# Optimization experiments

Hardware: AMD Instinct MI355X
Metric: run time of the kernel (lower is better)

The kernel has to match this reference:

```python
import jax, jax.numpy as jnp
import numpy as np

B, S, D = 4, 2048, 2048
H, G, HD = 16, 4, 128  # n_heads, kv groups, head_dim
EPS = 1e-6


def setup_inputs() -> dict:
    key = jax.random.key(0)
    ks = jax.random.split(key, 8)
    x = jax.random.normal(ks[0], (B, S, D), dtype=jnp.float32)
    # causal mask, True = attend (already 'inverted' for SDPA semantics)
    mask = jnp.tril(jnp.ones((S, S), dtype=bool))
    # RoPE tables: (S, HD), rotate-half convention with duplicated freqs
    inv_freq = 1.0 / (10000.0 ** (np.arange(0, HD, 2, dtype=np.float32) / HD))
    ang = np.arange(S, dtype=np.float32)[:, None] * inv_freq[None, :]  # (S, HD/2)
    ang = np.concatenate([ang, ang], axis=-1)  # (S, HD)
    cos = jnp.asarray(np.cos(ang))
    sin = jnp.asarray(np.sin(ang))
    s = 0.02
    wq = jax.random.normal(ks[1], (D, H * HD), dtype=jnp.float32) * s
    wk = jax.random.normal(ks[2], (D, G * HD), dtype=jnp.float32) * s
    wv = jax.random.normal(ks[3], (D, G * HD), dtype=jnp.float32) * s
    wg = jax.random.normal(ks[4], (D, H * HD), dtype=jnp.float32) * s
    wo = jax.random.normal(ks[5], (H * HD, D), dtype=jnp.float32) * s
    q_scale = jax.random.normal(ks[6], (HD,), dtype=jnp.float32) * 0.01  # zero-centered
    k_scale = jax.random.normal(ks[7], (HD,), dtype=jnp.float32) * 0.01
    return dict(x=x, mask=mask, cos=cos, sin=sin, wq=wq, wk=wk, wv=wv,
                wg=wg, wo=wo, q_scale=q_scale, k_scale=k_scale)


def _zc_rmsnorm(x, scale):
    # zero-centered RMSNorm in fp32: x * rsqrt(mean(x^2)+eps) * (1+scale)
    xf = x.astype(jnp.float32)
    rms = jax.lax.rsqrt(jnp.mean(xf * xf, axis=-1, keepdims=True) + EPS)
    return (xf * rms * (1.0 + scale)).astype(x.dtype)


def _rope(x, cos, sin):
    # x: (b, h, s, hd); cos/sin: (s, hd)
    hd = x.shape[-1]
    x1, x2 = x[..., : hd // 2], x[..., hd // 2 :]
    rot = jnp.concatenate([-x2, x1], axis=-1)
    return x * cos[None, None] + rot * sin[None, None]


def reference(x, mask, cos, sin, wq, wk, wv, wg, wo, q_scale, k_scale):
    b, s, d = x.shape
    q = (x @ wq).reshape(b, s, H, HD).transpose(0, 2, 1, 3)   # (b,H,s,hd)
    k = (x @ wk).reshape(b, s, G, HD).transpose(0, 2, 1, 3)   # (b,G,s,hd)
    v = (x @ wv).reshape(b, s, G, HD).transpose(0, 2, 1, 3)
    gate = jax.nn.sigmoid(x @ wg)                              # (b,s,H*HD)

    q = _rope(_zc_rmsnorm(q, q_scale), cos, sin)
    k = _rope(_zc_rmsnorm(k, k_scale), cos, sin)

    rep = H // G
    k = jnp.repeat(k, rep, axis=1)   # (b,H,s,hd)
    v = jnpep = jnp.repeat(v, rep, axis=1) if False else jnp.repeat(v, rep, axis=1)

    scores = jnp.einsum('bhqd,bhkd->bhqk', q, k) / jnp.sqrt(jnp.float32(HD))
    scores = jnp.where(mask[None, None, :s, :s], scores, jnp.float32(-1e30))
    attn = jax.nn.softmax(scores, axis=-1)
    ctx = jnp.einsum('bhqk,bhkd->bhqd', attn, v)               # (b,H,s,hd)
    ctx = ctx.transpose(0, 2, 1, 3).reshape(b, s, H * HD)
    return (ctx * gate) @ wo
```

## Files before the change

kernel.cpp:

```cpp
#include <hip/hip_runtime.h>

typedef __bf16 bf16;
typedef __attribute__((ext_vector_type(8))) __bf16 bf16x8;
typedef __attribute__((ext_vector_type(4))) float f32x4;

constexpr int Bb = 4, S = 2048, Dd = 2048, H = 16, G = 4, HD = 128;
constexpr float L2E = 1.4426950408889634f;

__device__ inline f32x4 mfma16(bf16x8 a, bf16x8 b, f32x4 c) {
  return __builtin_amdgcn_mfma_f32_16x16x32_bf16(a, b, c, 0, 0, 0);
}

__device__ inline void gl_lds16(const void* g, void* l) {
  __builtin_amdgcn_global_load_lds(
      (const __attribute__((address_space(1))) void*)g,
      (__attribute__((address_space(3))) void*)l, 16, 0, 0);
}

__global__ __launch_bounds__(256) void k_f32_to_bf16(
    const float* __restrict__ in, bf16* __restrict__ out, int n8) {
  int i = blockIdx.x * 256 + threadIdx.x;
  if (i >= n8) return;
  const float4* p = (const float4*)(in + (long long)i * 8);
  float4 a = p[0], b = p[1];
  bf16x8 v;
  v[0] = (bf16)a.x; v[1] = (bf16)a.y; v[2] = (bf16)a.z; v[3] = (bf16)a.w;
  v[4] = (bf16)b.x; v[5] = (bf16)b.y; v[6] = (bf16)b.z; v[7] = (bf16)b.w;
  *(bf16x8*)(out + (long long)i * 8) = v;
}

__global__ __launch_bounds__(256) void k_wtrans(
    const float* __restrict__ wq, const float* __restrict__ wk,
    const float* __restrict__ wv, const float* __restrict__ wg,
    const float* __restrict__ wo, bf16* __restrict__ wcat,
    bf16* __restrict__ woT) {
  __shared__ float tile[32][33];
  const int z = blockIdx.z;
  const float* src;
  bf16* dst;
  int C;
  switch (z) {
    case 0: src = wq; C = 2048; dst = wcat; break;
    case 1: src = wk; C = 512; dst = wcat + (long long)2048 * 2048; break;
    case 2: src = wv; C = 512; dst = wcat + (long long)2560 * 2048; break;
    case 3: src = wg; C = 2048; dst = wcat + (long long)3072 * 2048; break;
    default: src = wo; C = 2048; dst = woT; break;
  }
  int c0 = blockIdx.x * 32, r0 = blockIdx.y * 32;
  if (c0 >= C) return;
  int tx = threadIdx.x, ty = threadIdx.y;
#pragma unroll
  for (int i = 0; i < 4; ++i) {
    int r = r0 + ty + i * 8, c = c0 + tx;
    tile[ty + i * 8][tx] = (c < C) ? src[(long long)r * C + c] : 0.f;
  }
  __syncthreads();
#pragma unroll
  for (int i = 0; i < 4; ++i) {
    int c = c0 + ty + i * 8, r = r0 + tx;
    if (c < C) dst[(long long)c * 2048 + r] = (bf16)tile[tx][ty + i * 8];
  }
}

template <typename InT>
__global__ __launch_bounds__(256) void k_transpose_bf16(
    const InT* __restrict__ in, long long s1, int nb2, long long s2, int ldin,
    bf16* __restrict__ out, long long obatch, int ldout, int R, int C) {
  __shared__ float tile[32][33];
  int z = blockIdx.z;
  const InT* ip = in + (long long)(z / nb2) * s1 + (long long)(z % nb2) * s2;
  bf16* op = out + (long long)z * obatch;
  int c0 = blockIdx.x * 32, r0 = blockIdx.y * 32;
  int tx = threadIdx.x, ty = threadIdx.y;
#pragma unroll
  for (int i = 0; i < 4; ++i) {
    int r = r0 + ty + i * 8, c = c0 + tx;
    tile[ty + i * 8][tx] = (r < R && c < C) ? (float)ip[(long long)r * ldin + c] : 0.f;
  }
  __syncthreads();
#pragma unroll
  for (int i = 0; i < 4; ++i) {
    int c = c0 + ty + i * 8, r = r0 + tx;
    if (c < C && r < R) op[(long long)c * ldout + r] = (bf16)tile[tx][ty + i * 8];
  }
}

template <typename CT, bool SIG>
__global__ __launch_bounds__(512, 1) void k_gemm256(
    const bf16* __restrict__ A, int lda, const bf16* __restrict__ Bt, int ldb,
    CT* __restrict__ C, int ldc, int M, int N, int K, int sig_from) {
  __shared__ bf16 ldsbuf[65536];
  char* lds2 = (char*)ldsbuf;
  const int tid = threadIdx.x;
  const int w = tid >> 6, lane = tid & 63;
  const int l16 = lane & 15, lh = lane >> 4;
  const int wr = w >> 2, wc = w & 3;
  const int nbn = N >> 8;
  const int cpx = gridDim.x >> 3;
  const int swz = (blockIdx.x & 7) * cpx + (blockIdx.x >> 3);
  const int bm = swz / nbn, bn = swz % nbn;
  const int m0 = bm << 8, n0 = bn << 8;

  const int lrow = lane >> 3;
  const int lcol = ((lane & 7) ^ lrow) * 8;
  const int arb = wr * 128 + wc * 16;
  const int xg = wc >> 1, sg = wr * 2 + (wc & 1);
  const int brb = xg * 128 + (sg >> 1) * 64 + (sg & 1) * 16;
  const bf16* aS0 = A + (long long)(m0 + arb + lrow) * lda + lcol;
  const bf16* aS1 = A + (long long)(m0 + arb + 8 + lrow) * lda + lcol;
  const bf16* bS0 = Bt + (long long)(n0 + brb + lrow) * ldb + lcol;
  const bf16* bS1 = Bt + (long long)(n0 + brb + 8 + lrow) * ldb + lcol;

  auto stageA = [&](int buf, int k0, int hi) {
    k0 = (k0 < K) ? k0 : 0;
    gl_lds16(aS0 + (long long)hi * 64 * lda + k0,
             lds2 + buf * 65536 + (arb + hi * 64) * 128);
    gl_lds16(aS1 + (long long)hi * 64 * lda + k0,
             lds2 + buf * 65536 + (arb + hi * 64 + 8) * 128);
  };
  auto stageB = [&](int buf, int k0, int hi) {
    k0 = (k0 < K) ? k0 : 0;
    gl_lds16(bS0 + (long long)hi * 32 * ldb + k0,
             lds2 + buf * 65536 + 32768 + (brb + hi * 32) * 128);
    gl_lds16(bS1 + (long long)hi * 32 * ldb + k0,
             lds2 + buf * 65536 + 32768 + (brb + hi * 32 + 8) * 128);
  };

  const int swzc = (l16 & 7) << 4;
  auto rdA = [&](bf16x8 (&dst)[4][2], const char* L, int mh) {
#pragma unroll
    for (int m = 0; m < 4; ++m)
#pragma unroll
      for (int ks = 0; ks < 2; ++ks)
        dst[m][ks] = *(const bf16x8*)(L + (wr * 128 + mh * 64 + m * 16 + l16) * 128 +
                                      ((ks * 64 + lh * 16) ^ swzc));
  };
  auto rdB = [&](bf16x8 (&dst)[2][2], const char* L, int nh) {
#pragma unroll
    for (int n = 0; n < 2; ++n)
#pragma unroll
      for (int ks = 0; ks < 2; ++ks)
        dst[n][ks] = *(const bf16x8*)(L + 32768 + (wc * 64 + nh * 32 + n * 16 + l16) * 128 +
                                      ((ks * 64 + lh * 16) ^ swzc));
  };

  f32x4 acc[8][4] = {};
  bf16x8 aflo[4][2], afhi[4][2], bn0[2][2], bn1[2][2];
  const int NT = K >> 6;

  stageA(0, 0, 0);
  stageB(0, 0, 0);
  stageB(0, 0, 1);
  stageA(0, 0, 1);
  stageA(1, 64, 0);
  asm volatile("s_waitcnt vmcnt(4)" ::: "memory");
  __builtin_amdgcn_s_barrier();
  asm volatile("" ::: "memory");
  rdA(aflo, lds2, 0);
  rdB(bn0, lds2, 0);

  for (int t = 0; t < NT; ++t) {
    const int buf = t & 1, nb = buf ^ 1;
    const char* L = lds2 + buf * 65536;
    const char* Ln = lds2 + nb * 65536;
    const int k1 = (t + 1) << 6;
    const bool more = (t + 1 < NT);
    stageB(nb, k1, 0);
    rdB(bn1, L, 1);
    __builtin_amdgcn_s_setprio(1);
#pragma unroll
    for (int ks = 0; ks < 2; ++ks)
#pragma unroll
      for (int m = 0; m < 4; ++m)
#pragma unroll
        for (int n = 0; n < 2; ++n)
          acc[m][n] = mfma16(aflo[m][ks], bn0[n][ks], acc[m][n]);
    __builtin_amdgcn_s_setprio(0);
    asm volatile("s_waitcnt vmcnt(4)" ::: "memory");
    __builtin_amdgcn_s_barrier();
    asm volatile("" ::: "memory");
    stageB(nb, k1, 1);
    rdA(afhi, L, 1);
    __builtin_amdgcn_s_setprio(1);
#pragma unroll
    for (int ks = 0; ks < 2; ++ks)
#pragma unroll
      for (int m = 0; m < 4; ++m)
#pragma unroll
        for (int n = 0; n < 2; ++n)
          acc[m][2 + n] = mfma16(aflo[m][ks], bn1[n][ks], acc[m][2 + n]);
    __builtin_amdgcn_s_setprio(0);
    __builtin_amdgcn_s_barrier();
    asm volatile("" ::: "memory");
    stageA(nb, k1, 1);
    __builtin_amdgcn_s_setprio(1);
#pragma unroll
    for (int ks = 0; ks < 2; ++ks)
#pragma unroll
      for (int m = 0; m < 4; ++m)
#pragma unroll
        for (int n = 0; n < 2; ++n)
          acc[4 + m][2 + n] = mfma16(afhi[m][ks], bn1[n][ks], acc[4 + m][2 + n]);
    __builtin_amdgcn_s_setprio(0);
    asm volatile("s_waitcnt vmcnt(4)" ::: "memory");
    __builtin_amdgcn_s_barrier();
    asm volatile("" ::: "memory");
    if (more) rdA(aflo, Ln, 0);
    stageA(buf, (t + 2) << 6, 0);
    __builtin_amdgcn_s_setprio(1);
#pragma unroll
    for (int ks = 0; ks < 2; ++ks)
#pragma unroll
      for (int m = 0; m < 4; ++m)
#pragma unroll
        for (int n = 0; n < 2; ++n)
          acc[4 + m][n] = mfma16(afhi[m][ks], bn0[n][ks], acc[4 + m][n]);
    __builtin_amdgcn_s_setprio(0);
    if (more) rdB(bn0, Ln, 0);
    asm volatile("s_waitcnt vmcnt(4)" ::: "memory");
    __builtin_amdgcn_s_barrier();
    asm volatile("" ::: "memory");
  }

#pragma unroll
  for (int m = 0; m < 8; ++m)
#pragma unroll
    for (int n = 0; n < 4; ++n) {
      const int col = n0 + wc * 64 + n * 16 + l16;
#pragma unroll
      for (int r = 0; r < 4; ++r) {
        float v = acc[m][n][r];
        if (SIG && col >= sig_from) v = 1.f / (1.f + exp2f(-v * L2E));
        C[(long long)(m0 + wr * 128 + m * 16 + lh * 4 + r) * ldc + col] = (CT)v;
      }
    }
}

__global__ __launch_bounds__(256) void k_rms_rope2(
    const bf16* __restrict__ C1, const float* __restrict__ qs,
    const float* __restrict__ ksc, const float* __restrict__ cosT,
    const float* __restrict__ sinT, bf16* __restrict__ qb,
    bf16* __restrict__ kb) {
  int wid = (blockIdx.x * 256 + threadIdx.x) >> 6;
  int lane = threadIdx.x & 63;
  const bf16* ip;
  const float* scale;
  bf16* op;
  float oscale;
  int s;
  if (wid < 131072) {
    int h = wid & 15, bs = wid >> 4;
    s = bs & 2047;
    int b = bs >> 11;
    ip = C1 + (long long)bs * 5120 + h * HD;
    scale = qs;
    oscale = 0.12751879523209308f;
    op = qb + (((long long)b * H + h) * S + s) * HD;
  } else {
    wid -= 131072;
    int h = wid & 3, bs = wid >> 2;
    s = bs & 2047;
    int b = bs >> 11;
    ip = C1 + 2048 + (long long)bs * 5120 + h * HD;
    scale = ksc;
    oscale = 1.0f;
    op = kb + (((long long)b * G + h) * S + s) * HD;
  }
  float x1 = (float)ip[lane], x2 = (float)ip[lane + 64];
  float ss = x1 * x1 + x2 * x2;
#pragma unroll
  for (int m = 1; m < 64; m <<= 1) ss += __shfl_xor(ss, m);
  float rms = rsqrtf(ss * (1.f / 128.f) + 1e-6f);
  float n1 = x1 * rms * (1.f + scale[lane]);
  float n2 = x2 * rms * (1.f + scale[lane + 64]);
  float o1 = (n1 * cosT[s * 128 + lane] - n2 * sinT[s * 128 + lane]) * oscale;
  float o2 = (n2 * cosT[s * 128 + lane + 64] + n1 * sinT[s * 128 + lane + 64]) * oscale;
  op[lane] = (bf16)o1;
  op[lane + 64] = (bf16)o2;
}

__global__ __launch_bounds__(512, 2) void k_flash3(
    const bf16* __restrict__ Q, const bf16* __restrict__ Kb,
    const bf16* __restrict__ Vt, const bf16* __restrict__ gate, int ldg,
    bf16* __restrict__ outc, int ldo) {
  __shared__ bf16 Ks[2][64 * 128];
  __shared__ bf16 Vs[128 * 64];
  __shared__ bf16 Ps[8][32 * 64];
  const int tid = threadIdx.x, w = tid >> 6, lane = tid & 63;
  const int l16 = lane & 15, lh = lane >> 4;
  const int bh = blockIdx.x & 63;
  const int qi = blockIdx.x >> 6;
  const int qc = 7 - qi;
  const int h = bh & 15, b = bh >> 4, g = h >> 2;
  const int qbase = qc * 256;
  const int q0w = qbase + w * 32;
  const bf16* qp = Q + (((long long)b * H + h) * S + q0w) * HD;
  const bf16* kp = Kb + ((long long)b * G + g) * S * HD;
  const bf16* vp = Vt + ((long long)b * G + g) * (long long)HD * S;

  bf16x8 aq[2][4];
#pragma unroll
  for (int m = 0; m < 2; ++m)
#pragma unroll
    for (int ks = 0; ks < 4; ++ks)
      aq[m][ks] = *(const bf16x8*)(qp + (long long)(m * 16 + l16) * HD + ks * 32 + lh * 8);

  f32x4 acc[2][8] = {};
  float mrow[2][4], lrow[2][4];
#pragma unroll
  for (int m = 0; m < 2; ++m)
#pragma unroll
    for (int r = 0; r < 4; ++r) { mrow[m][r] = -1e30f; lrow[m][r] = 0.f; }

  const int ntiles = qc * 4 + 4;

  auto stageK = [&](int bi, int t) {
    const int kv0 = t << 6;
#pragma unroll
    for (int i = 0; i < 2; ++i) {
      int c = w * 128 + i * 64 + lane;
      int row = c >> 4;
      int cb = ((c & 15) << 4) ^ ((row & 7) << 4);
      gl_lds16(kp + (long long)(kv0 + row) * HD + (cb >> 1),
               (char*)Ks[bi] + (w * 128 + i * 64) * 16);
    }
  };
  auto stageV = [&](int t) {
    const int kv0 = t << 6;
#pragma unroll
    for (int i = 0; i < 2; ++i) {
      int c = w * 128 + i * 64 + lane;
      int rowv = c >> 3;
      int cbv = ((c & 7) << 4) ^ ((rowv & 7) << 4);
      gl_lds16(vp + (long long)rowv * S + kv0 + (cbv >> 1),
               (char*)Vs + (w * 128 + i * 64) * 16);
    }
  };

  stageK(0, 0);
  asm volatile("s_waitcnt vmcnt(0)" ::: "memory");
  __builtin_amdgcn_s_barrier();
  asm volatile("" ::: "memory");

  for (int t = 0; t < ntiles; ++t) {
    const int buf = t & 1;
    const int kv0 = t << 6;
    const bool active = (kv0 <= q0w + 31);
    stageV(t);
    if (t + 1 < ntiles) stageK(buf ^ 1, t + 1);
    if (active) {
      f32x4 s[2][4] = {};
#pragma unroll
      for (int ks = 0; ks < 4; ++ks)
#pragma unroll
        for (int n = 0; n < 4; ++n) {
          int row = n * 16 + l16;
          int off = row * 256 + ((ks * 64 + lh * 16) ^ ((row & 7) << 4));
          bf16x8 kb = *(const bf16x8*)((const char*)Ks[buf] + off);
#pragma unroll
          for (int m = 0; m < 2; ++m) s[m][n] = mfma16(aq[m][ks], kb, s[m][n]);
        }
      if (kv0 + 63 > q0w) {
#pragma unroll
        for (int m = 0; m < 2; ++m)
#pragma unroll
          for (int n = 0; n < 4; ++n)
#pragma unroll
            for (int r = 0; r < 4; ++r) {
              int col = kv0 + n * 16 + l16;
              int rowg = q0w + m * 16 + lh * 4 + r;
              if (col > rowg) s[m][n][r] = -1e30f;
            }
      }
      float lm[2][4];
      bool okl = true;
#pragma unroll
      for (int m = 0; m < 2; ++m)
#pragma unroll
        for (int r = 0; r < 4; ++r) {
          lm[m][r] = fmaxf(fmaxf(s[m][0][r], s[m][1][r]), fmaxf(s[m][2][r], s[m][3][r]));
          okl = okl && (lm[m][r] <= mrow[m][r] + 8.f);
        }
      if (!__all(okl)) {
#pragma unroll
        for (int st = 1; st < 16; st <<= 1)
#pragma unroll
          for (int m = 0; m < 2; ++m)
#pragma unroll
            for (int r = 0; r < 4; ++r) lm[m][r] = fmaxf(lm[m][r], __shfl_xor(lm[m][r], st));
#pragma unroll
        for (int m = 0; m < 2; ++m)
#pragma unroll
          for (int r = 0; r < 4; ++r) {
            float mn = fmaxf(mrow[m][r], lm[m][r]);
            float resc = exp2f(mrow[m][r] - mn);
            mrow[m][r] = mn;
            lrow[m][r] *= resc;
#pragma unroll
            for (int dt = 0; dt < 8; ++dt) acc[m][dt][r] *= resc;
          }
      }
#pragma unroll
      for (int m = 0; m < 2; ++m)
#pragma unroll
        for (int n = 0; n < 4; ++n)
#pragma unroll
          for (int r = 0; r < 4; ++r) {
            float p = exp2f(s[m][n][r] - mrow[m][r]);
            s[m][n][r] = p;
            int row = m * 16 + lh * 4 + r;
            *(bf16*)((char*)Ps[w] + row * 128 +
                     ((n * 32 + l16 * 2) ^ ((row & 7) << 4))) = (bf16)p;
          }
#pragma unroll
      for (int m = 0; m < 2; ++m)
#pragma unroll
        for (int r = 0; r < 4; ++r)
          lrow[m][r] += s[m][0][r] + s[m][1][r] + s[m][2][r] + s[m][3][r];
    }
    asm volatile("s_waitcnt vmcnt(2)" ::: "memory");
    __builtin_amdgcn_s_barrier();
    asm volatile("" ::: "memory");
    if (active) {
      bf16x8 pa[2][2];
#pragma unroll
      for (int m = 0; m < 2; ++m)
#pragma unroll
        for (int kf = 0; kf < 2; ++kf) {
          int row = m * 16 + l16;
          pa[m][kf] = *(const bf16x8*)((const char*)Ps[w] + row * 128 +
                                       ((kf * 64 + lh * 16) ^ ((row & 7) << 4)));
        }
#pragma unroll
      for (int kf = 0; kf < 2; ++kf)
#pragma unroll
        for (int dt = 0; dt < 8; ++dt) {
          int d = dt * 16 + l16;
          int off = d * 128 + ((kf * 64 + lh * 16) ^ ((d & 7) << 4));
          bf16x8 vb = *(const bf16x8*)((const char*)Vs + off);
#pragma unroll
          for (int m = 0; m < 2; ++m) acc[m][dt] = mfma16(pa[m][kf], vb, acc[m][dt]);
        }
    }
    asm volatile("s_waitcnt vmcnt(0)" ::: "memory");
    __builtin_amdgcn_s_barrier();
    asm volatile("" ::: "memory");
  }

#pragma unroll
  for (int st = 1; st < 16; st <<= 1)
#pragma unroll
    for (int m = 0; m < 2; ++m)
#pragma unroll
      for (int r = 0; r < 4; ++r) lrow[m][r] += __shfl_xor(lrow[m][r], st);
  float inv[2][4];
#pragma unroll
  for (int m = 0; m < 2; ++m)
#pragma unroll
    for (int r = 0; r < 4; ++r) inv[m][r] = 1.f / lrow[m][r];
#pragma unroll
  for (int m = 0; m < 2; ++m)
#pragma unroll
    for (int dt = 0; dt < 8; ++dt)
#pragma unroll
      for (int r = 0; r < 4; ++r) {
        int rowg = q0w + m * 16 + lh * 4 + r;
        long long row = (long long)b * S + rowg;
        int col = h * HD + dt * 16 + l16;
        float gv = (float)gate[row * ldg + col];
        outc[row * ldo + col] = (bf16)(acc[m][dt][r] * inv[m][r] * gv);
      }
}

extern "C" void kernel_launch(void* const* d_in, const int* in_sizes, int n_in,
                              void* d_out, int out_size, void* d_ws, size_t ws_size,
                              hipStream_t stream) {
  const float* x = (const float*)d_in[0];
  const float* cosT = (const float*)d_in[2];
  const float* sinT = (const float*)d_in[3];
  const float* wq = (const float*)d_in[4];
  const float* wk = (const float*)d_in[5];
  const float* wv = (const float*)d_in[6];
  const float* wg = (const float*)d_in[7];
  const float* wo = (const float*)d_in[8];
  const float* qs = (const float*)d_in[9];
  const float* ksc = (const float*)d_in[10];
  float* out = (float*)d_out;
  char* ws = (char*)d_ws;

  if (ws_size < 146800640) return;
  bf16* xb = (bf16*)(ws);
  bf16* wcat = (bf16*)(ws + 33554432);
  bf16* woT = (bf16*)(ws + 54525952);
  bf16* C1 = (bf16*)(ws + 62914560);
  bf16* qbuf = xb;
  bf16* kbuf = wcat;
  bf16* vtbuf = wcat + 4194304;
  bf16* gatep = C1 + 3072;
  bf16* ctxg = C1;

  dim3 tb(32, 8);
  k_f32_to_bf16<<<8192, 256, 0, stream>>>(x, xb, Bb * S * Dd / 8);
  k_wtrans<<<dim3(64, 64, 5), tb, 0, stream>>>(wq, wk, wv, wg, wo, wcat, woT);
  k_gemm256<bf16, true><<<32 * 20, 512, 0, stream>>>(
      xb, 2048, wcat, 2048, C1, 5120, 8192, 5120, 2048, 3072);
  k_rms_rope2<<<40960, 256, 0, stream>>>(C1, qs, ksc, cosT, sinT, qbuf, kbuf);
  k_transpose_bf16<bf16><<<dim3(4, 64, 16), tb, 0, stream>>>(
      C1 + 2560, (long long)2048 * 5120, 4, 128, 5120, vtbuf,
      (long long)128 * 2048, 2048, 2048, 128);
  k_flash3<<<512, 512, 0, stream>>>(qbuf, kbuf, vtbuf, gatep, 5120, ctxg, 5120);
  k_gemm256<float, false><<<32 * 8, 512, 0, stream>>>(
      ctxg, 5120, woT, 2048, out, 2048, 8192, 2048, 2048, 1 << 30);
}
```

Measured before the change: 443.2 us.

## Restructure GEMM main loop into unrolled two-tile ping-pong with explicit LDS waits

Rewrites the 256x256 bf16 GEMM K-loop as a macro-expanded stage sequence, unrolled by two so the LDS buffer offsets are compile-time constants. It also reorders the global-to-LDS stage issue, LDS fragment reads and barriers, using lgkmcnt waits and sched_barrier to separate memory phases from MFMA clusters. The aim is to cut per-iteration address arithmetic and branches and to overlap loads with MFMA work more tightly. The tail handling assumes an even tile count of at least two, and the added barriers and waits could stall the waves.

```diff
diff --git a/kernel.cpp b/kernel.cpp
--- a/kernel.cpp
+++ b/kernel.cpp
@@ -111,116 +111,116 @@
   const bf16* bS0 = Bt + (long long)(n0 + brb + lrow) * ldb + lcol;
   const bf16* bS1 = Bt + (long long)(n0 + brb + 8 + lrow) * ldb + lcol;
 
-  auto stageA = [&](int buf, int k0, int hi) {
-    k0 = (k0 < K) ? k0 : 0;
+  auto stageA = [&](int bufoff, int k0, int hi) {
     gl_lds16(aS0 + (long long)hi * 64 * lda + k0,
-             lds2 + buf * 65536 + (arb + hi * 64) * 128);
+             lds2 + bufoff + (arb + hi * 64) * 128);
     gl_lds16(aS1 + (long long)hi * 64 * lda + k0,
-             lds2 + buf * 65536 + (arb + hi * 64 + 8) * 128);
-  };
-  auto stageB = [&](int buf, int k0, int hi) {
-    k0 = (k0 < K) ? k0 : 0;
+             lds2 + bufoff + (arb + hi * 64 + 8) * 128);
+  };
+  auto stageB = [&](int bufoff, int k0, int hi) {
     gl_lds16(bS0 + (long long)hi * 32 * ldb + k0,
-             lds2 + buf * 65536 + 32768 + (brb + hi * 32) * 128);
+             lds2 + bufoff + 32768 + (brb + hi * 32) * 128);
     gl_lds16(bS1 + (long long)hi * 32 * ldb + k0,
-             lds2 + buf * 65536 + 32768 + (brb + hi * 32 + 8) * 128);
+             lds2 + bufoff + 32768 + (brb + hi * 32 + 8) * 128);
   };
 
   const int swzc = (l16 & 7) << 4;
-  auto rdA = [&](bf16x8 (&dst)[4][2], const char* L, int mh) {
+  auto rdA = [&](bf16x8 (&dst)[4][2], int bufoff, int mh) {
 #pragma unroll
     for (int m = 0; m < 4; ++m)
 #pragma unroll
       for (int ks = 0; ks < 2; ++ks)
-        dst[m][ks] = *(const bf16x8*)(L + (wr * 128 + mh * 64 + m * 16 + l16) * 128 +
+        dst[m][ks] = *(const bf16x8*)(lds2 + bufoff +
+                                      (wr * 128 + mh * 64 + m * 16 + l16) * 128 +
                                       ((ks * 64 + lh * 16) ^ swzc));
   };
-  auto rdB = [&](bf16x8 (&dst)[2][2], const char* L, int nh) {
+  auto rdB = [&](bf16x8 (&dst)[2][2], int bufoff, int nh) {
 #pragma unroll
     for (int n = 0; n < 2; ++n)
 #pragma unroll
       for (int ks = 0; ks < 2; ++ks)
-        dst[n][ks] = *(const bf16x8*)(L + 32768 + (wc * 64 + nh * 32 + n * 16 + l16) * 128 +
+        dst[n][ks] = *(const bf16x8*)(lds2 + bufoff + 32768 +
+                                      (wc * 64 + nh * 32 + n * 16 + l16) * 128 +
                                       ((ks * 64 + lh * 16) ^ swzc));
   };
 
   f32x4 acc[8][4] = {};
   bf16x8 aflo[4][2], afhi[4][2], bn0[2][2], bn1[2][2];
+
+  auto mmc = [&](const bf16x8 (&AF)[4][2], const bf16x8 (&BF)[2][2], int MB, int NB) {
+#pragma unroll
+    for (int ks = 0; ks < 2; ++ks)
+#pragma unroll
+      for (int m = 0; m < 4; ++m)
+#pragma unroll
+        for (int n = 0; n < 2; ++n)
+          acc[MB + m][NB + n] = mfma16(AF[m][ks], BF[n][ks], acc[MB + m][NB + n]);
+  };
+
   const int NT = K >> 6;
+
+#define KTILE(CUR, NXT, KA, KB)                                         \
+  {                                                                     \
+                      \
+    rdA(aflo, CUR, 0);                                                  \
+    rdB(bn0, CUR, 0);                                                   \
+    stageB(NXT, KA, 1);                                                 \
+    asm volatile("s_waitcnt lgkmcnt(8)" ::: "memory");                  \
+    __builtin_amdgcn_s_barrier();                                       \
+    asm volatile("s_waitcnt lgkmcnt(0)" ::: "memory");                  \
+    __builtin_amdgcn_sched_barrier(0);                                  \
+    __builtin_amdgcn_s_setprio(1);                                      \
+    mmc(aflo, bn0, 0, 0);                                               \
+    __builtin_amdgcn_s_setprio(0);                                      \
+    __builtin_amdgcn_s_barrier();                                       \
+                            \
+    rdB(bn1, CUR, 1);                                                   \
+    stageA(NXT, KA, 1);                                                 \
+    __builtin_amdgcn_s_barrier();                                       \
+    asm volatile("s_waitcnt lgkmcnt(0)" ::: "memory");                  \
+    __builtin_amdgcn_sched_barrier(0);                                  \
+    __builtin_amdgcn_s_setprio(1);                                      \
+    mmc(aflo, bn1, 0, 2);                                               \
+    __builtin_amdgcn_s_setprio(0);                                      \
+    __builtin_amdgcn_s_barrier();                                       \
+                           \
+    rdA(afhi, CUR, 1);                                                  \
+    stageA(CUR, KB, 0);                                                 \
+    __builtin_amdgcn_s_barrier();                                       \
+    asm volatile("s_waitcnt lgkmcnt(0)" ::: "memory");                  \
+    __builtin_amdgcn_sched_barrier(0);                                  \
+    __builtin_amdgcn_s_setprio(1);                                      \
+    mmc(afhi, bn1, 4, 2);                                               \
+    __builtin_amdgcn_s_setprio(0);                                      \
+    __builtin_amdgcn_s_barrier();                                       \
+         \
+    stageB(CUR, KB, 0);                                                 \
+    __builtin_amdgcn_s_barrier();                                       \
+    __builtin_amdgcn_sched_barrier(0);                                  \
+    __builtin_amdgcn_s_setprio(1);                                      \
+    mmc(afhi, bn0, 4, 0);                                               \
+    __builtin_amdgcn_s_setprio(0);                                      \
+    asm volatile("s_waitcnt vmcnt(4)" ::: "memory");                    \
+    __builtin_amdgcn_s_barrier();                                       \
+  }
 
   stageA(0, 0, 0);
   stageB(0, 0, 0);
   stageB(0, 0, 1);
   stageA(0, 0, 1);
-  stageA(1, 64, 0);
+  stageA(65536, 64, 0);
+  stageB(65536, 64, 0);
   asm volatile("s_waitcnt vmcnt(4)" ::: "memory");
   __builtin_amdgcn_s_barrier();
-  asm volatile("" ::: "memory");
-  rdA(aflo, lds2, 0);
-  rdB(bn0, lds2, 0);
-
-  for (int t = 0; t < NT; ++t) {
-    const int buf = t & 1, nb = buf ^ 1;
-    const char* L = lds2 + buf * 65536;
-    const char* Ln = lds2 + nb * 65536;
-    const int k1 = (t + 1) << 6;
-    const bool more = (t + 1 < NT);
-    stageB(nb, k1, 0);
-    rdB(bn1, L, 1);
-    __builtin_amdgcn_s_setprio(1);
-#pragma unroll
-    for (int ks = 0; ks < 2; ++ks)
-#pragma unroll
-      for (int m = 0; m < 4; ++m)
-#pragma unroll
-        for (int n = 0; n < 2; ++n)
-          acc[m][n] = mfma16(aflo[m][ks], bn0[n][ks], acc[m][n]);
-    __builtin_amdgcn_s_setprio(0);
-    asm volatile("s_waitcnt vmcnt(4)" ::: "memory");
-    __builtin_amdgcn_s_barrier();
-    asm volatile("" ::: "memory");
-    stageB(nb, k1, 1);
-    rdA(afhi, L, 1);
-    __builtin_amdgcn_s_setprio(1);
-#pragma unroll
-    for (int ks = 0; ks < 2; ++ks)
-#pragma unroll
-      for (int m = 0; m < 4; ++m)
-#pragma unroll
-        for (int n = 0; n < 2; ++n)
-          acc[m][2 + n] = mfma16(aflo[m][ks], bn1[n][ks], acc[m][2 + n]);
-    __builtin_amdgcn_s_setprio(0);
-    __builtin_amdgcn_s_barrier();
-    asm volatile("" ::: "memory");
-    stageA(nb, k1, 1);
-    __builtin_amdgcn_s_setprio(1);
-#pragma unroll
-    for (int ks = 0; ks < 2; ++ks)
-#pragma unroll
-      for (int m = 0; m < 4; ++m)
-#pragma unroll
-        for (int n = 0; n < 2; ++n)
-          acc[4 + m][2 + n] = mfma16(afhi[m][ks], bn1[n][ks], acc[4 + m][2 + n]);
-    __builtin_amdgcn_s_setprio(0);
-    asm volatile("s_waitcnt vmcnt(4)" ::: "memory");
-    __builtin_amdgcn_s_barrier();
-    asm volatile("" ::: "memory");
-    if (more) rdA(aflo, Ln, 0);
-    stageA(buf, (t + 2) << 6, 0);
-    __builtin_amdgcn_s_setprio(1);
-#pragma unroll
-    for (int ks = 0; ks < 2; ++ks)
-#pragma unroll
-      for (int m = 0; m < 4; ++m)
-#pragma unroll
-        for (int n = 0; n < 2; ++n)
-          acc[4 + m][n] = mfma16(afhi[m][ks], bn0[n][ks], acc[4 + m][n]);
-    __builtin_amdgcn_s_setprio(0);
-    if (more) rdB(bn0, Ln, 0);
-    asm volatile("s_waitcnt vmcnt(4)" ::: "memory");
-    __builtin_amdgcn_s_barrier();
-    asm volatile("" ::: "memory");
-  }
+
+  int t = 0;
+  for (; t + 3 < NT; t += 2) {
+    KTILE(0, 65536, (t + 1) << 6, (t + 2) << 6)
+    KTILE(65536, 0, (t + 2) << 6, (t + 3) << 6)
+  }
+  KTILE(0, 65536, (NT - 1) << 6, 0)
+  KTILE(65536, 0, 0, 0)
+#undef KTILE
 
 #pragma unroll
   for (int m = 0; m < 8; ++m)
```

After: 456.3 us. 3.0% more time.

## Fuse RMSNorm and RoPE into QKV GEMM epilogue, read Q/K in place

Applied to the files above, without the earlier changes.

Removes the separate RMSNorm+RoPE kernel. The projection GEMM now normalises and rotates its Q and K tiles in the epilogue, swapping the two 64-column head halves between paired warps through LDS and reducing the sum of squares with lane shuffles. The flash-attention kernel reads Q and K directly from the strided projection buffer and writes the gated context back into the Q region. It also always issues the next K stage load, presumably to keep the vmcnt-based waits consistent. This saves one full read/write pass over Q/K and a launch, at the cost of a heavier GEMM epilogue with an extra barrier and strided attention loads.

```diff
diff --git a/kernel.cpp b/kernel.cpp
--- a/kernel.cpp
+++ b/kernel.cpp
@@ -85,10 +85,12 @@
   }
 }
 
-template <typename CT, bool SIG>
+template <typename CT, bool SIG, bool FUSE>
 __global__ __launch_bounds__(512, 1) void k_gemm256(
     const bf16* __restrict__ A, int lda, const bf16* __restrict__ Bt, int ldb,
-    CT* __restrict__ C, int ldc, int M, int N, int K, int sig_from) {
+    CT* __restrict__ C, int ldc, int M, int N, int K, int sig_from,
+    const float* __restrict__ qsp, const float* __restrict__ ksp,
+    const float* __restrict__ cosTp, const float* __restrict__ sinTp) {
   __shared__ bf16 ldsbuf[65536];
   char* lds2 = (char*)ldsbuf;
   const int tid = threadIdx.x;
@@ -222,6 +224,69 @@
     asm volatile("" ::: "memory");
   }
 
+  if (FUSE && n0 < 2560) {
+    const bool isQ = (n0 < 2048);
+    const float osc = isQ ? 0.12751879523209308f : 1.0f;
+    const float* sct = isQ ? qsp : ksp;
+    const int dbase = (wc & 1) * 64;
+    float sc_own[4], sc_pair[4];
+#pragma unroll
+    for (int n = 0; n < 4; ++n) {
+      int d = dbase + n * 16 + l16;
+      sc_own[n] = 1.f + sct[d];
+      sc_pair[n] = 1.f + sct[d ^ 64];
+    }
+    char* myx = lds2 + w * 16384;
+#pragma unroll
+    for (int m = 0; m < 8; ++m)
+#pragma unroll
+      for (int n = 0; n < 4; ++n)
+#pragma unroll
+        for (int r = 0; r < 4; ++r) {
+          int row = m * 16 + lh * 4 + r;
+          int cb = ((n * 16 + l16) * 2) ^ ((row & 7) << 4);
+          *(bf16*)(myx + row * 128 + cb) = (bf16)acc[m][n][r];
+        }
+    __syncthreads();
+    const char* px = lds2 + (w ^ 1) * 16384;
+    const float sgn = (wc & 1) ? 1.f : -1.f;
+#pragma unroll
+    for (int m = 0; m < 8; ++m) {
+      float pvv[4][4];
+      float ss[4] = {0.f, 0.f, 0.f, 0.f};
+#pragma unroll
+      for (int n = 0; n < 4; ++n)
+#pragma unroll
+        for (int r = 0; r < 4; ++r) {
+          int row = m * 16 + lh * 4 + r;
+          int cb = ((n * 16 + l16) * 2) ^ ((row & 7) << 4);
+          float pv = (float)*(const bf16*)(px + row * 128 + cb);
+          float ov = (float)(bf16)acc[m][n][r];
+          pvv[n][r] = pv;
+          acc[m][n][r] = ov;
+          ss[r] += ov * ov + pv * pv;
+        }
+#pragma unroll
+      for (int mask = 1; mask < 16; mask <<= 1)
+#pragma unroll
+        for (int r = 0; r < 4; ++r) ss[r] += __shfl_xor(ss[r], mask);
+#pragma unroll
+      for (int r = 0; r < 4; ++r) {
+        float rms = rsqrtf(ss[r] * 0.0078125f + 1e-6f);
+        int rglob = m0 + wr * 128 + m * 16 + lh * 4 + r;
+        const float* ct = cosTp + (long long)(rglob & 2047) * 128;
+        const float* st = sinTp + (long long)(rglob & 2047) * 128;
+#pragma unroll
+        for (int n = 0; n < 4; ++n) {
+          int d = dbase + n * 16 + l16;
+          float o = (acc[m][n][r] * sc_own[n] * ct[d] +
+                     sgn * pvv[n][r] * sc_pair[n] * st[d]) * rms * osc;
+          C[(long long)rglob * ldc + n0 + wc * 64 + n * 16 + l16] = (CT)o;
+        }
+      }
+    }
+    return;
+  }
 #pragma unroll
   for (int m = 0; m < 8; ++m)
 #pragma unroll
@@ -236,53 +301,8 @@
     }
 }
 
-__global__ __launch_bounds__(256) void k_rms_rope2(
-    const bf16* __restrict__ C1, const float* __restrict__ qs,
-    const float* __restrict__ ksc, const float* __restrict__ cosT,
-    const float* __restrict__ sinT, bf16* __restrict__ qb,
-    bf16* __restrict__ kb) {
-  int wid = (blockIdx.x * 256 + threadIdx.x) >> 6;
-  int lane = threadIdx.x & 63;
-  const bf16* ip;
-  const float* scale;
-  bf16* op;
-  float oscale;
-  int s;
-  if (wid < 131072) {
-    int h = wid & 15, bs = wid >> 4;
-    s = bs & 2047;
-    int b = bs >> 11;
-    ip = C1 + (long long)bs * 5120 + h * HD;
-    scale = qs;
-    oscale = 0.12751879523209308f;
-    op = qb + (((long long)b * H + h) * S + s) * HD;
-  } else {
-    wid -= 131072;
-    int h = wid & 3, bs = wid >> 2;
-    s = bs & 2047;
-    int b = bs >> 11;
-    ip = C1 + 2048 + (long long)bs * 5120 + h * HD;
-    scale = ksc;
-    oscale = 1.0f;
-    op = kb + (((long long)b * G + h) * S + s) * HD;
-  }
-  float x1 = (float)ip[lane], x2 = (float)ip[lane + 64];
-  float ss = x1 * x1 + x2 * x2;
-#pragma unroll
-  for (int m = 1; m < 64; m <<= 1) ss += __shfl_xor(ss, m);
-  float rms = rsqrtf(ss * (1.f / 128.f) + 1e-6f);
-  float n1 = x1 * rms * (1.f + scale[lane]);
-  float n2 = x2 * rms * (1.f + scale[lane + 64]);
-  float o1 = (n1 * cosT[s * 128 + lane] - n2 * sinT[s * 128 + lane]) * oscale;
-  float o2 = (n2 * cosT[s * 128 + lane + 64] + n1 * sinT[s * 128 + lane + 64]) * oscale;
-  op[lane] = (bf16)o1;
-  op[lane + 64] = (bf16)o2;
-}
-
 __global__ __launch_bounds__(512, 2) void k_flash3(
-    const bf16* __restrict__ Q, const bf16* __restrict__ Kb,
-    const bf16* __restrict__ Vt, const bf16* __restrict__ gate, int ldg,
-    bf16* __restrict__ outc, int ldo) {
+    bf16* __restrict__ C1p, const bf16* __restrict__ Vt) {
   __shared__ bf16 Ks[2][64 * 128];
   __shared__ bf16 Vs[128 * 64];
   __shared__ bf16 Ps[8][32 * 64];
@@ -292,18 +312,18 @@
   const int qi = blockIdx.x >> 6;
   const int qc = 7 - qi;
   const int h = bh & 15, b = bh >> 4, g = h >> 2;
-  const int qbase = qc * 256;
-  const int q0w = qbase + w * 32;
-  const bf16* qp = Q + (((long long)b * H + h) * S + q0w) * HD;
-  const bf16* kp = Kb + ((long long)b * G + g) * S * HD;
+  const int q0w = qc * 256 + w * 32;
+  const bf16* qp = C1p + (long long)(b * 2048 + q0w) * 5120 + h * 128;
+  const bf16* kp = C1p + (long long)(b * 2048) * 5120 + 2048 + g * 128;
   const bf16* vp = Vt + ((long long)b * G + g) * (long long)HD * S;
+  const bf16* gatep = C1p + 3072;
 
   bf16x8 aq[2][4];
 #pragma unroll
   for (int m = 0; m < 2; ++m)
 #pragma unroll
     for (int ks = 0; ks < 4; ++ks)
-      aq[m][ks] = *(const bf16x8*)(qp + (long long)(m * 16 + l16) * HD + ks * 32 + lh * 8);
+      aq[m][ks] = *(const bf16x8*)(qp + (long long)(m * 16 + l16) * 5120 + ks * 32 + lh * 8);
 
   f32x4 acc[2][8] = {};
   float mrow[2][4], lrow[2][4];
@@ -321,7 +341,7 @@
       int c = w * 128 + i * 64 + lane;
       int row = c >> 4;
       int cb = ((c & 15) << 4) ^ ((row & 7) << 4);
-      gl_lds16(kp + (long long)(kv0 + row) * HD + (cb >> 1),
+      gl_lds16(kp + (long long)(kv0 + row) * 5120 + (cb >> 1),
                (char*)Ks[bi] + (w * 128 + i * 64) * 16);
     }
   };
@@ -347,7 +367,7 @@
     const int kv0 = t << 6;
     const bool active = (kv0 <= q0w + 31);
     stageV(t);
-    if (t + 1 < ntiles) stageK(buf ^ 1, t + 1);
+    stageK(buf ^ 1, (t + 1 < ntiles) ? t + 1 : t);
     if (active) {
       f32x4 s[2][4] = {};
 #pragma unroll
@@ -467,8 +487,8 @@
         int rowg = q0w + m * 16 + lh * 4 + r;
         long long row = (long long)b * S + rowg;
         int col = h * HD + dt * 16 + l16;
-        float gv = (float)gate[row * ldg + col];
-        outc[row * ldo + col] = (bf16)(acc[m][dt][r] * inv[m][r] * gv);
+        float gv = (float)gatep[row * 5120 + col];
+        C1p[row * 5120 + col] = (bf16)(acc[m][dt][r] * inv[m][r] * gv);
       }
 }
 
@@ -493,22 +513,19 @@
   bf16* wcat = (bf16*)(ws + 33554432);
   bf16* woT = (bf16*)(ws + 54525952);
   bf16* C1 = (bf16*)(ws + 62914560);
-  bf16* qbuf = xb;
-  bf16* kbuf = wcat;
   bf16* vtbuf = wcat + 4194304;
-  bf16* gatep = C1 + 3072;
   bf16* ctxg = C1;
 
   dim3 tb(32, 8);
   k_f32_to_bf16<<<8192, 256, 0, stream>>>(x, xb, Bb * S * Dd / 8);
   k_wtrans<<<dim3(64, 64, 5), tb, 0, stream>>>(wq, wk, wv, wg, wo, wcat, woT);
-  k_gemm256<bf16, true><<<32 * 20, 512, 0, stream>>>(
-      xb, 2048, wcat, 2048, C1, 5120, 8192, 5120, 2048, 3072);
-  k_rms_rope2<<<40960, 256, 0, stream>>>(C1, qs, ksc, cosT, sinT, qbuf, kbuf);
+  k_gemm256<bf16, true, true><<<32 * 20, 512, 0, stream>>>(
+      xb, 2048, wcat, 2048, C1, 5120, 8192, 5120, 2048, 3072, qs, ksc, cosT, sinT);
   k_transpose_bf16<bf16><<<dim3(4, 64, 16), tb, 0, stream>>>(
       C1 + 2560, (long long)2048 * 5120, 4, 128, 5120, vtbuf,
       (long long)128 * 2048, 2048, 2048, 128);
-  k_flash3<<<512, 512, 0, stream>>>(qbuf, kbuf, vtbuf, gatep, 5120, ctxg, 5120);
-  k_gemm256<float, false><<<32 * 8, 512, 0, stream>>>(
-      ctxg, 5120, woT, 2048, out, 2048, 8192, 2048, 2048, 1 << 30);
-}
+  k_flash3<<<512, 512, 0, stream>>>(C1, vtbuf);
+  k_gemm256<float, false, false><<<32 * 8, 512, 0, stream>>>(
+      ctxg, 5120, woT, 2048, out, 2048, 8192, 2048, 2048, 1 << 30,
+      nullptr, nullptr, nullptr, nullptr);
+}
```

After: 462.9 us. 1.04x slower.
